# Performance work log

Measured on AMD Instinct MI355X. Metric: run time of the kernel, lower is better.

## Reference

```python
import jax, jax.numpy as jnp
import numpy as np

N = 100000      # nodes
DEG = 16        # in-degree per node
E = N * DEG     # edges
IN_DIM = 128
OUT_DIM = 32
EPS = 1e-8      # torch cosine_similarity norm clamp


def setup_inputs() -> dict:
    key = jax.random.key(0)
    k1, k2, k3, k4 = jax.random.split(key, 4)
    h = jax.random.normal(k1, (N, IN_DIM), dtype=jnp.float32)
    # xavier_uniform-scaled linear weight, shape [out_dim, in_dim] like nn.Linear
    W = jax.random.normal(k2, (OUT_DIM, IN_DIM), dtype=jnp.float32) * (1.0 / np.sqrt(IN_DIM))
    beta = jax.random.uniform(k3, (1,), dtype=jnp.float32)
    src = jax.random.randint(k4, (E,), 0, N)
    dst = jnp.arange(E) // DEG  # each node gets exactly DEG incoming edges
    return {"h": h, "W": W, "beta": beta, "src": src, "dst": dst}


def reference(h, W, beta, src, dst):
    # Note: F.dropout(p=0.6) from the original is omitted for a deterministic reference.
    z = h @ W.T                                   # [N, out_dim]
    zs = z[src]                                   # [E, out_dim] gather src features
    zd = z[dst]                                   # [E, out_dim] gather dst features
    num = jnp.sum(zs * zd, axis=-1)               # [E]
    ns = jnp.maximum(jnp.linalg.norm(zs, axis=-1), EPS)
    nd = jnp.maximum(jnp.linalg.norm(zd, axis=-1), EPS)
    cos = num / (ns * nd)                         # torch.cosine_similarity
    e = -beta[0] * (1.0 - cos)                    # [E] edge score
    # segment softmax over incoming edges of each dst node (stable)
    m = jax.ops.segment_max(e, dst, num_segments=N)
    m = jnp.where(jnp.isfinite(m), m, 0.0)        # guard isolated nodes
    ex = jnp.exp(e - m[dst])                      # [E]
    denom = jax.ops.segment_sum(ex, dst, num_segments=N)
    alpha = ex / denom[dst]                       # [E] attention weights
    # weighted scatter-sum of src features to dst nodes
    return jax.ops.segment_sum(alpha[:, None] * zs, dst, num_segments=N)  # [N, out_dim]
```

## Files before the change

kernel.cpp:

```cpp
#include <hip/hip_runtime.h>

#define IN_DIM 128
#define OUT_DIM 32
#define DEG 16
#define EPS 1e-8f

typedef __attribute__((ext_vector_type(8))) short bf16x8;
typedef __attribute__((ext_vector_type(4))) float f32x4;

#define SWZ(x, p) __int_as_float(__builtin_amdgcn_ds_swizzle(__float_as_int(x), (p)))

static __device__ __forceinline__ unsigned short f2bf(float x) {
  unsigned u = __float_as_uint(x);
  u += 0x7FFFu + ((u >> 16) & 1u);
  return (unsigned short)(u >> 16);
}
static __device__ __forceinline__ float bflo(unsigned u) { return __uint_as_float(u << 16); }
static __device__ __forceinline__ float bfhi(unsigned u) { return __uint_as_float(u & 0xFFFF0000u); }

static __device__ __forceinline__ bf16x8 pack8(float4 a, float4 b) {
  bf16x8 r;
  r[0] = (short)f2bf(a.x); r[1] = (short)f2bf(a.y);
  r[2] = (short)f2bf(a.z); r[3] = (short)f2bf(a.w);
  r[4] = (short)f2bf(b.x); r[5] = (short)f2bf(b.y);
  r[6] = (short)f2bf(b.z); r[7] = (short)f2bf(b.w);
  return r;
}

__global__ __launch_bounds__(256) void gemm_norm_kernel(
    const float* __restrict__ h, const float* __restrict__ W,
    unsigned short* __restrict__ zhb, float* __restrict__ nrm, int N) {
  const int tid = threadIdx.x;
  const int wv = tid >> 6;
  const int l = tid & 63;
  const int n16 = l & 15;
  const int q = l >> 4;
  const int mb = (blockIdx.x * 4 + wv) * 16;
  if (mb >= N) return;

  bf16x8 bfr[2][4];
#pragma unroll
  for (int oh = 0; oh < 2; ++oh) {
    const float* wr = W + (size_t)(oh * 16 + n16) * IN_DIM + q * 8;
#pragma unroll
    for (int c = 0; c < 4; ++c)
      bfr[oh][c] = pack8(*(const float4*)(wr + c * 32),
                         *(const float4*)(wr + c * 32 + 4));
  }
  int m = mb + n16;
  if (m >= N) m = N - 1;
  bf16x8 afr[4];
  {
    const float* hr = h + (size_t)m * IN_DIM + q * 8;
#pragma unroll
    for (int c = 0; c < 4; ++c)
      afr[c] = pack8(*(const float4*)(hr + c * 32),
                     *(const float4*)(hr + c * 32 + 4));
  }

  f32x4 acc0 = {0.f, 0.f, 0.f, 0.f}, acc1 = {0.f, 0.f, 0.f, 0.f};
#pragma unroll
  for (int c = 0; c < 4; ++c) {
    acc0 = __builtin_amdgcn_mfma_f32_16x16x32_bf16(afr[c], bfr[0][c], acc0, 0, 0, 0);
    acc1 = __builtin_amdgcn_mfma_f32_16x16x32_bf16(afr[c], bfr[1][c], acc1, 0, 0, 0);
  }

#pragma unroll
  for (int r = 0; r < 4; ++r) {
    float s = acc0[r] * acc0[r] + acc1[r] * acc1[r];
    s += SWZ(s, 0x041F);
    s += SWZ(s, 0x081F);
    s += SWZ(s, 0x101F);
    s += SWZ(s, 0x201F);
    const float ns = sqrtf(s);
    const float inv = 1.0f / fmaxf(ns, EPS);
    const float z0 = acc0[r] * inv, z1 = acc1[r] * inv;
    const float p0 = SWZ(z0, 0x041F), p1 = SWZ(z1, 0x041F);
    const int node = mb + q * 4 + r;
    if (((n16 & 1) == 0) && node < N) {
      unsigned short* zr = zhb + (size_t)node * OUT_DIM;
      *(unsigned*)(zr + n16) =
          (unsigned)f2bf(z0) | ((unsigned)f2bf(p0) << 16);
      *(unsigned*)(zr + 16 + n16) =
          (unsigned)f2bf(z1) | ((unsigned)f2bf(p1) << 16);
    }
    if (n16 == 0 && node < N) nrm[node] = ns;
  }
}

__global__ __launch_bounds__(256) void edge_kernel(
    const unsigned short* __restrict__ zhb, const float* __restrict__ nrm,
    const int* __restrict__ src, const float* __restrict__ beta_p,
    float* __restrict__ out, int N) {
  __shared__ float xp[8 * DEG * 36];

  const int tid = threadIdx.x;
  const int l5 = tid & 31, half = (tid >> 5) & 1, wv = tid >> 6;
  const int gw = blockIdx.x * 4 + wv;
  if (gw * 2 >= N) return;
  const int n = gw * 2 + half;
  const int ne = (n < N) ? n : N - 1;
  const int e = l5 >> 1, c = l5 & 1;

  const float beta = *beta_p;
  const int se = src[(size_t)ne * DEG + e];
  const float nrm_s = nrm[se];

  const uint4* zs4 = (const uint4*)(zhb + (size_t)se * OUT_DIM) + c * 2;
  const uint4 sa = zs4[0], sb = zs4[1];
  const uint4* zd4 = (const uint4*)(zhb + (size_t)ne * OUT_DIM) + c * 2;
  const uint4 da = zd4[0], db = zd4[1];

  float vs[16];
  vs[0] = bflo(sa.x);  vs[1] = bfhi(sa.x);  vs[2] = bflo(sa.y);  vs[3] = bfhi(sa.y);
  vs[4] = bflo(sa.z);  vs[5] = bfhi(sa.z);  vs[6] = bflo(sa.w);  vs[7] = bfhi(sa.w);
  vs[8] = bflo(sb.x);  vs[9] = bfhi(sb.x);  vs[10] = bflo(sb.y); vs[11] = bfhi(sb.y);
  vs[12] = bflo(sb.z); vs[13] = bfhi(sb.z); vs[14] = bflo(sb.w); vs[15] = bfhi(sb.w);
  float vd[16];
  vd[0] = bflo(da.x);  vd[1] = bfhi(da.x);  vd[2] = bflo(da.y);  vd[3] = bfhi(da.y);
  vd[4] = bflo(da.z);  vd[5] = bfhi(da.z);  vd[6] = bflo(da.w);  vd[7] = bfhi(da.w);
  vd[8] = bflo(db.x);  vd[9] = bfhi(db.x);  vd[10] = bflo(db.y); vd[11] = bfhi(db.y);
  vd[12] = bflo(db.z); vd[13] = bfhi(db.z); vd[14] = bflo(db.w); vd[15] = bfhi(db.w);

  float pr = vs[0] * vd[0];
#pragma unroll
  for (int i = 1; i < 16; ++i) pr = fmaf(vs[i], vd[i], pr);
  pr += SWZ(pr, 0x041F);

  const float ex = __expf(beta * (pr - 1.0f));

  float den = ex;
  den += SWZ(den, 0x081F);
  den += SWZ(den, 0x101F);
  den += SWZ(den, 0x201F);
  den += SWZ(den, 0x401F);
  const float rd = 1.0f / den;

  const float sc = ex * nrm_s;
  float* slot = xp + (wv * 2 + half) * (DEG * 36);
  float4* wp = (float4*)(slot + e * 36 + c * 16);
  wp[0] = make_float4(sc * vs[0], sc * vs[1], sc * vs[2], sc * vs[3]);
  wp[1] = make_float4(sc * vs[4], sc * vs[5], sc * vs[6], sc * vs[7]);
  wp[2] = make_float4(sc * vs[8], sc * vs[9], sc * vs[10], sc * vs[11]);
  wp[3] = make_float4(sc * vs[12], sc * vs[13], sc * vs[14], sc * vs[15]);

  float s = 0.f;
#pragma unroll
  for (int e2 = 0; e2 < DEG; ++e2)
    s += slot[e2 * 36 + l5];

  if (n < N) out[(size_t)n * OUT_DIM + l5] = s * rd;
}

extern "C" void kernel_launch(void* const* d_in, const int* in_sizes, int n_in,
                              void* d_out, int out_size, void* d_ws, size_t ws_size,
                              hipStream_t stream) {
  const float* h    = (const float*)d_in[0];
  const float* W    = (const float*)d_in[1];
  const float* beta = (const float*)d_in[2];
  const int*   src  = (const int*)d_in[3];

  const int N = in_sizes[0] / IN_DIM;

  unsigned short* zhb = (unsigned short*)d_ws;
  float* nrm = (float*)(zhb + (size_t)N * OUT_DIM);

  const int bl1 = (N + 63) / 64;
  gemm_norm_kernel<<<bl1, 256, 0, stream>>>(h, W, zhb, nrm, N);

  const int bl2 = (N + 7) / 8;
  edge_kernel<<<bl2, 256, 0, stream>>>(zhb, nrm, src, beta, (float*)d_out, N);
}
```

Before: 131.7 us.

## Make edge kernel persistent with software-prefetched gathers across grid-stride iterations

The edge kernel becomes a grid-stride persistent loop with the grid capped at 2048 blocks. Each wave loads source indices two groups ahead and the bf16 source/destination feature rows plus norms one group ahead, so gather latency overlaps with the current group's dot product, softmax and LDS reduction. The aim is to hide the dependent index→feature load chain, at the cost of more registers and fewer resident blocks, which could reduce latency hiding from wave parallelism.

```diff
diff --git a/kernel.cpp b/kernel.cpp
--- a/kernel.cpp
+++ b/kernel.cpp
@@ -96,60 +96,97 @@
 
   const int tid = threadIdx.x;
   const int l5 = tid & 31, half = (tid >> 5) & 1, wv = tid >> 6;
-  const int gw = blockIdx.x * 4 + wv;
-  if (gw * 2 >= N) return;
-  const int n = gw * 2 + half;
-  const int ne = (n < N) ? n : N - 1;
   const int e = l5 >> 1, c = l5 & 1;
-
   const float beta = *beta_p;
-  const int se = src[(size_t)ne * DEG + e];
-  const float nrm_s = nrm[se];
-
-  const uint4* zs4 = (const uint4*)(zhb + (size_t)se * OUT_DIM) + c * 2;
-  const uint4 sa = zs4[0], sb = zs4[1];
-  const uint4* zd4 = (const uint4*)(zhb + (size_t)ne * OUT_DIM) + c * 2;
-  const uint4 da = zd4[0], db = zd4[1];
-
-  float vs[16];
-  vs[0] = bflo(sa.x);  vs[1] = bfhi(sa.x);  vs[2] = bflo(sa.y);  vs[3] = bfhi(sa.y);
-  vs[4] = bflo(sa.z);  vs[5] = bfhi(sa.z);  vs[6] = bflo(sa.w);  vs[7] = bfhi(sa.w);
-  vs[8] = bflo(sb.x);  vs[9] = bfhi(sb.x);  vs[10] = bflo(sb.y); vs[11] = bfhi(sb.y);
-  vs[12] = bflo(sb.z); vs[13] = bfhi(sb.z); vs[14] = bflo(sb.w); vs[15] = bfhi(sb.w);
-  float vd[16];
-  vd[0] = bflo(da.x);  vd[1] = bfhi(da.x);  vd[2] = bflo(da.y);  vd[3] = bfhi(da.y);
-  vd[4] = bflo(da.z);  vd[5] = bfhi(da.z);  vd[6] = bflo(da.w);  vd[7] = bfhi(da.w);
-  vd[8] = bflo(db.x);  vd[9] = bfhi(db.x);  vd[10] = bflo(db.y); vd[11] = bfhi(db.y);
-  vd[12] = bflo(db.z); vd[13] = bfhi(db.z); vd[14] = bflo(db.w); vd[15] = bfhi(db.w);
-
-  float pr = vs[0] * vd[0];
-#pragma unroll
-  for (int i = 1; i < 16; ++i) pr = fmaf(vs[i], vd[i], pr);
-  pr += SWZ(pr, 0x041F);
-
-  const float ex = __expf(beta * (pr - 1.0f));
-
-  float den = ex;
-  den += SWZ(den, 0x081F);
-  den += SWZ(den, 0x101F);
-  den += SWZ(den, 0x201F);
-  den += SWZ(den, 0x401F);
-  const float rd = 1.0f / den;
-
-  const float sc = ex * nrm_s;
   float* slot = xp + (wv * 2 + half) * (DEG * 36);
-  float4* wp = (float4*)(slot + e * 36 + c * 16);
-  wp[0] = make_float4(sc * vs[0], sc * vs[1], sc * vs[2], sc * vs[3]);
-  wp[1] = make_float4(sc * vs[4], sc * vs[5], sc * vs[6], sc * vs[7]);
-  wp[2] = make_float4(sc * vs[8], sc * vs[9], sc * vs[10], sc * vs[11]);
-  wp[3] = make_float4(sc * vs[12], sc * vs[13], sc * vs[14], sc * vs[15]);
-
-  float s = 0.f;
-#pragma unroll
-  for (int e2 = 0; e2 < DEG; ++e2)
-    s += slot[e2 * 36 + l5];
-
-  if (n < N) out[(size_t)n * OUT_DIM + l5] = s * rd;
+
+  const int ngrp = (N + 1) >> 1;
+  const int gstep = (int)gridDim.x * 4;
+  int g = blockIdx.x * 4 + wv;
+  if (g >= ngrp) return;
+
+  int n0 = g * 2 + half;
+  int ne0 = (n0 < N) ? n0 : N - 1;
+  int se0 = src[(size_t)ne0 * DEG + e];
+  float nrm0 = nrm[se0];
+  const uint4* p0 = (const uint4*)(zhb + (size_t)se0 * OUT_DIM) + c * 2;
+  uint4 sa = p0[0], sb = p0[1];
+  const uint4* q0 = (const uint4*)(zhb + (size_t)ne0 * OUT_DIM) + c * 2;
+  uint4 da = q0[0], db = q0[1];
+
+  int g1 = g + gstep;
+  int se1 = 0, n1 = 0, ne1 = 0;
+  if (g1 < ngrp) {
+    n1 = g1 * 2 + half;
+    ne1 = (n1 < N) ? n1 : N - 1;
+    se1 = src[(size_t)ne1 * DEG + e];
+  }
+
+  for (;;) {
+    const int g2 = g1 + gstep;
+    int se2 = 0, n2 = 0, ne2 = 0;
+    if (g2 < ngrp) {
+      n2 = g2 * 2 + half;
+      ne2 = (n2 < N) ? n2 : N - 1;
+      se2 = src[(size_t)ne2 * DEG + e];
+    }
+
+    float vs[16];
+    vs[0] = bflo(sa.x);  vs[1] = bfhi(sa.x);  vs[2] = bflo(sa.y);  vs[3] = bfhi(sa.y);
+    vs[4] = bflo(sa.z);  vs[5] = bfhi(sa.z);  vs[6] = bflo(sa.w);  vs[7] = bfhi(sa.w);
+    vs[8] = bflo(sb.x);  vs[9] = bfhi(sb.x);  vs[10] = bflo(sb.y); vs[11] = bfhi(sb.y);
+    vs[12] = bflo(sb.z); vs[13] = bfhi(sb.z); vs[14] = bflo(sb.w); vs[15] = bfhi(sb.w);
+    float vd[16];
+    vd[0] = bflo(da.x);  vd[1] = bfhi(da.x);  vd[2] = bflo(da.y);  vd[3] = bfhi(da.y);
+    vd[4] = bflo(da.z);  vd[5] = bfhi(da.z);  vd[6] = bflo(da.w);  vd[7] = bfhi(da.w);
+    vd[8] = bflo(db.x);  vd[9] = bfhi(db.x);  vd[10] = bflo(db.y); vd[11] = bfhi(db.y);
+    vd[12] = bflo(db.z); vd[13] = bfhi(db.z); vd[14] = bflo(db.w); vd[15] = bfhi(db.w);
+
+    float pr = vs[0] * vd[0];
+#pragma unroll
+    for (int i = 1; i < 16; ++i) pr = fmaf(vs[i], vd[i], pr);
+    pr += SWZ(pr, 0x041F);
+
+    const float ex = __expf(beta * (pr - 1.0f));
+
+    float den = ex;
+    den += SWZ(den, 0x081F);
+    den += SWZ(den, 0x101F);
+    den += SWZ(den, 0x201F);
+    den += SWZ(den, 0x401F);
+    const float rd = 1.0f / den;
+    const float sc = ex * nrm0;
+
+    const bool more = (g1 < ngrp);
+    uint4 sa_n, sb_n, da_n, db_n;
+    float nrm_n = 0.f;
+    if (more) {
+      nrm_n = nrm[se1];
+      const uint4* p1 = (const uint4*)(zhb + (size_t)se1 * OUT_DIM) + c * 2;
+      sa_n = p1[0]; sb_n = p1[1];
+      const uint4* q1 = (const uint4*)(zhb + (size_t)ne1 * OUT_DIM) + c * 2;
+      da_n = q1[0]; db_n = q1[1];
+    }
+
+    float4* wp = (float4*)(slot + e * 36 + c * 16);
+    wp[0] = make_float4(sc * vs[0], sc * vs[1], sc * vs[2], sc * vs[3]);
+    wp[1] = make_float4(sc * vs[4], sc * vs[5], sc * vs[6], sc * vs[7]);
+    wp[2] = make_float4(sc * vs[8], sc * vs[9], sc * vs[10], sc * vs[11]);
+    wp[3] = make_float4(sc * vs[12], sc * vs[13], sc * vs[14], sc * vs[15]);
+
+    float s = 0.f;
+#pragma unroll
+    for (int e2 = 0; e2 < DEG; ++e2)
+      s += slot[e2 * 36 + l5];
+
+    if (n0 < N) out[(size_t)n0 * OUT_DIM + l5] = s * rd;
+
+    if (!more) break;
+    n0 = n1;
+    nrm0 = nrm_n;
+    sa = sa_n; sb = sb_n; da = da_n; db = db_n;
+    g1 = g2; n1 = n2; ne1 = ne2; se1 = se2;
+  }
 }
 
 extern "C" void kernel_launch(void* const* d_in, const int* in_sizes, int n_in,
@@ -168,6 +205,8 @@
   const int bl1 = (N + 63) / 64;
   gemm_norm_kernel<<<bl1, 256, 0, stream>>>(h, W, zhb, nrm, N);
 
-  const int bl2 = (N + 7) / 8;
+  const int ngrp = (N + 1) / 2;
+  int bl2 = (ngrp + 3) / 4;
+  if (bl2 > 2048) bl2 = 2048;
   edge_kernel<<<bl2, 256, 0, stream>>>(zhb, nrm, src, beta, (float*)d_out, N);
 }
```

Measured after the change: 132.9 us. Within noise of the previous version (+0.9%).

## Assign one lane per edge in edge kernel, four nodes per wave

Applied to the files above, without the earlier changes.

Restructures the edge kernel so each lane processes an entire edge (all 32 features) instead of half an edge, and each wave covers four destination nodes instead of two. This removes the cross-lane swizzle for the dot product and halves the block count. The softmax sum now spans 16 lanes, and the final reduction reads and writes float2 per lane. The trade-off is higher register use per lane (64 unpacked floats) and twice the shared memory per block, which may lower occupancy for a gather-bound kernel.

```diff
diff --git a/kernel.cpp b/kernel.cpp
--- a/kernel.cpp
+++ b/kernel.cpp
@@ -25,6 +25,11 @@
   r[4] = (short)f2bf(b.x); r[5] = (short)f2bf(b.y);
   r[6] = (short)f2bf(b.z); r[7] = (short)f2bf(b.w);
   return r;
+}
+
+static __device__ __forceinline__ void unp8(uint4 u, float* p) {
+  p[0] = bflo(u.x); p[1] = bfhi(u.x); p[2] = bflo(u.y); p[3] = bfhi(u.y);
+  p[4] = bflo(u.z); p[5] = bfhi(u.z); p[6] = bflo(u.w); p[7] = bfhi(u.w);
 }
 
 __global__ __launch_bounds__(256) void gemm_norm_kernel(
@@ -92,64 +97,68 @@
     const unsigned short* __restrict__ zhb, const float* __restrict__ nrm,
     const int* __restrict__ src, const float* __restrict__ beta_p,
     float* __restrict__ out, int N) {
-  __shared__ float xp[8 * DEG * 36];
+  __shared__ float xp[16 * DEG * 36];
 
   const int tid = threadIdx.x;
-  const int l5 = tid & 31, half = (tid >> 5) & 1, wv = tid >> 6;
-  const int gw = blockIdx.x * 4 + wv;
-  if (gw * 2 >= N) return;
-  const int n = gw * 2 + half;
+  const int l = tid & 63, wv = tid >> 6;
+  const int e = l & 15;
+  const int nd = l >> 4;
+  const int base = (blockIdx.x * 4 + wv) * 4;
+  if (base >= N) return;
+  const int n = base + nd;
   const int ne = (n < N) ? n : N - 1;
-  const int e = l5 >> 1, c = l5 & 1;
 
   const float beta = *beta_p;
-  const int se = src[(size_t)ne * DEG + e];
+  const int se = src[(size_t)base * DEG + l];
   const float nrm_s = nrm[se];
 
-  const uint4* zs4 = (const uint4*)(zhb + (size_t)se * OUT_DIM) + c * 2;
-  const uint4 sa = zs4[0], sb = zs4[1];
-  const uint4* zd4 = (const uint4*)(zhb + (size_t)ne * OUT_DIM) + c * 2;
-  const uint4 da = zd4[0], db = zd4[1];
+  const uint4* zs4 = (const uint4*)(zhb + (size_t)se * OUT_DIM);
+  const uint4 s0 = zs4[0], s1 = zs4[1], s2 = zs4[2], s3 = zs4[3];
+  const uint4* zd4 = (const uint4*)(zhb + (size_t)ne * OUT_DIM);
+  const uint4 d0 = zd4[0], d1 = zd4[1], d2 = zd4[2], d3 = zd4[3];
 
-  float vs[16];
-  vs[0] = bflo(sa.x);  vs[1] = bfhi(sa.x);  vs[2] = bflo(sa.y);  vs[3] = bfhi(sa.y);
-  vs[4] = bflo(sa.z);  vs[5] = bfhi(sa.z);  vs[6] = bflo(sa.w);  vs[7] = bfhi(sa.w);
-  vs[8] = bflo(sb.x);  vs[9] = bfhi(sb.x);  vs[10] = bflo(sb.y); vs[11] = bfhi(sb.y);
-  vs[12] = bflo(sb.z); vs[13] = bfhi(sb.z); vs[14] = bflo(sb.w); vs[15] = bfhi(sb.w);
-  float vd[16];
-  vd[0] = bflo(da.x);  vd[1] = bfhi(da.x);  vd[2] = bflo(da.y);  vd[3] = bfhi(da.y);
-  vd[4] = bflo(da.z);  vd[5] = bfhi(da.z);  vd[6] = bflo(da.w);  vd[7] = bfhi(da.w);
-  vd[8] = bflo(db.x);  vd[9] = bfhi(db.x);  vd[10] = bflo(db.y); vd[11] = bfhi(db.y);
-  vd[12] = bflo(db.z); vd[13] = bfhi(db.z); vd[14] = bflo(db.w); vd[15] = bfhi(db.w);
+  float vs[32], vd[32];
+  unp8(s0, vs + 0); unp8(s1, vs + 8); unp8(s2, vs + 16); unp8(s3, vs + 24);
+  unp8(d0, vd + 0); unp8(d1, vd + 8); unp8(d2, vd + 16); unp8(d3, vd + 24);
 
-  float pr = vs[0] * vd[0];
+  float pa = vs[0] * vd[0], pb = vs[16] * vd[16];
 #pragma unroll
-  for (int i = 1; i < 16; ++i) pr = fmaf(vs[i], vd[i], pr);
-  pr += SWZ(pr, 0x041F);
+  for (int i = 1; i < 16; ++i) {
+    pa = fmaf(vs[i], vd[i], pa);
+    pb = fmaf(vs[16 + i], vd[16 + i], pb);
+  }
+  const float pr = pa + pb;
 
   const float ex = __expf(beta * (pr - 1.0f));
 
   float den = ex;
+  den += SWZ(den, 0x041F);
   den += SWZ(den, 0x081F);
   den += SWZ(den, 0x101F);
   den += SWZ(den, 0x201F);
-  den += SWZ(den, 0x401F);
   const float rd = 1.0f / den;
 
   const float sc = ex * nrm_s;
-  float* slot = xp + (wv * 2 + half) * (DEG * 36);
-  float4* wp = (float4*)(slot + e * 36 + c * 16);
-  wp[0] = make_float4(sc * vs[0], sc * vs[1], sc * vs[2], sc * vs[3]);
-  wp[1] = make_float4(sc * vs[4], sc * vs[5], sc * vs[6], sc * vs[7]);
-  wp[2] = make_float4(sc * vs[8], sc * vs[9], sc * vs[10], sc * vs[11]);
-  wp[3] = make_float4(sc * vs[12], sc * vs[13], sc * vs[14], sc * vs[15]);
 
-  float s = 0.f;
+  float* slot = xp + (wv * 4 + nd) * (DEG * 36) + e * 36;
+  float4* wp = (float4*)slot;
 #pragma unroll
-  for (int e2 = 0; e2 < DEG; ++e2)
-    s += slot[e2 * 36 + l5];
+  for (int q8 = 0; q8 < 8; ++q8)
+    wp[q8] = make_float4(sc * vs[4 * q8 + 0], sc * vs[4 * q8 + 1],
+                         sc * vs[4 * q8 + 2], sc * vs[4 * q8 + 3]);
 
-  if (n < N) out[(size_t)n * OUT_DIM + l5] = s * rd;
+  const float* rbase = xp + (wv * 4 + nd) * (DEG * 36) + 2 * e;
+  float ax = 0.f, ay = 0.f;
+#pragma unroll
+  for (int e2 = 0; e2 < DEG; ++e2) {
+    const float2 v = *(const float2*)(rbase + e2 * 36);
+    ax += v.x;
+    ay += v.y;
+  }
+
+  if (n < N) {
+    *(float2*)(out + (size_t)n * OUT_DIM + 2 * e) = make_float2(ax * rd, ay * rd);
+  }
 }
 
 extern "C" void kernel_launch(void* const* d_in, const int* in_sizes, int n_in,
@@ -168,6 +177,6 @@
   const int bl1 = (N + 63) / 64;
   gemm_norm_kernel<<<bl1, 256, 0, stream>>>(h, W, zhb, nrm, N);
 
-  const int bl2 = (N + 7) / 8;
+  const int bl2 = (N + 15) / 16;
   edge_kernel<<<bl2, 256, 0, stream>>>(zhb, nrm, src, beta, (float*)d_out, N);
 }
```

Result: slower. 135.0 us (+2.6%).
